# Kernel tuning notes

Measured on AMD Instinct MI355X. Metric: run time of the kernel, lower is better.

## Reference

```python
import jax, jax.numpy as jnp
import numpy as np

B, T, I, H = 32768, 18, 2, 64  # batch, seq_len (forced by fc2 in_features=18), input_dim, hidden_dim


def setup_inputs() -> dict:
    key = jax.random.key(0)
    ks = jax.random.split(key, 13)
    s = 1.0 / np.sqrt(H)  # torch default GRU/Linear init scale
    return {
        "x": jax.random.normal(ks[0], (B, T, I), jnp.float32),
        "w_ih_f": jax.random.uniform(ks[1], (3 * H, I), jnp.float32, -s, s),
        "w_hh_f": jax.random.uniform(ks[2], (3 * H, H), jnp.float32, -s, s),
        "b_ih_f": jax.random.uniform(ks[3], (3 * H,), jnp.float32, -s, s),
        "b_hh_f": jax.random.uniform(ks[4], (3 * H,), jnp.float32, -s, s),
        "w_ih_b": jax.random.uniform(ks[5], (3 * H, I), jnp.float32, -s, s),
        "w_hh_b": jax.random.uniform(ks[6], (3 * H, H), jnp.float32, -s, s),
        "b_ih_b": jax.random.uniform(ks[7], (3 * H,), jnp.float32, -s, s),
        "b_hh_b": jax.random.uniform(ks[8], (3 * H,), jnp.float32, -s, s),
        "fc1_w": jax.random.uniform(ks[9], (24, 2 * H), jnp.float32, -s, s),
        "fc1_b": jax.random.uniform(ks[10], (24,), jnp.float32, -s, s),
        "fc2_w": jax.random.uniform(ks[11], (2, T), jnp.float32, -s, s),
        "fc2_b": jax.random.uniform(ks[12], (2,), jnp.float32, -s, s),
    }


def _gru_scan(x_proj, w_hh, b_hh):
    """x_proj: (T, B, 3H) precomputed input projections. Returns (T, B, H)."""
    h0 = jnp.zeros((x_proj.shape[1], w_hh.shape[1]), x_proj.dtype)

    def step(h, xp):
        gh = h @ w_hh.T + b_hh
        i_r, i_z, i_n = jnp.split(xp, 3, axis=-1)
        h_r, h_z, h_n = jnp.split(gh, 3, axis=-1)
        r = jax.nn.sigmoid(i_r + h_r)
        z = jax.nn.sigmoid(i_z + h_z)
        n = jnp.tanh(i_n + r * h_n)
        h_new = (1 - z) * n + z * h
        return h_new, h_new

    _, hs = jax.lax.scan(step, h0, x_proj)
    return hs


def reference(x, w_ih_f, w_hh_f, b_ih_f, b_hh_f,
              w_ih_b, w_hh_b, b_ih_b, b_hh_b,
              fc1_w, fc1_b, fc2_w, fc2_b):
    # precompute input-gate projections for both directions: (T, B, 3H)
    xp_f = jnp.einsum('bti,gi->tbg', x, w_ih_f) + b_ih_f
    xp_b = jnp.einsum('bti,gi->tbg', x[:, ::-1], w_ih_b) + b_ih_b
    hf = _gru_scan(xp_f, w_hh_f, b_hh_f)           # (T, B, H)
    hb = _gru_scan(xp_b, w_hh_b, b_hh_b)[::-1]     # (T, B, H), re-aligned to forward time
    out = jnp.concatenate([hf, hb], axis=-1).transpose(1, 0, 2)  # (B, T, 2H)
    out = out @ fc1_w.T + fc1_b                    # (B, T, 24)
    out = out.reshape(out.shape[0], 24, -1)        # (B, 24, T) raw row-major reshape, as in torch
    out = out @ fc2_w.T + fc2_b                    # (B, 24, 2)
    return out
```

## Files before the change

kernel.cpp:

```cpp
#include <hip/hip_runtime.h>

#define TT 18

typedef __attribute__((ext_vector_type(8))) short short8;
typedef __attribute__((ext_vector_type(4))) float float4_t;
typedef __attribute__((ext_vector_type(2))) float float2_t;
typedef __attribute__((ext_vector_type(2))) unsigned int uint2_t;

static __device__ __forceinline__ float frcp(float x){ return __builtin_amdgcn_rcpf(x); }
static __device__ __forceinline__ float sigm(float x){ return frcp(1.f + __expf(-x)); }
static __device__ __forceinline__ float tanh_fast(float x){ return fmaf(2.f, frcp(1.f + __expf(-2.f*x)), -1.f); }
static __device__ __forceinline__ unsigned rne_bits(float f){
    unsigned u = __float_as_uint(f);
    return u + 0x7fffu + ((u >> 16) & 1u);
}
static __device__ __forceinline__ unsigned pack_hi16(unsigned hi_src, unsigned lo_src){
#if defined(__has_builtin)
#if __has_builtin(__builtin_amdgcn_perm)
    return __builtin_amdgcn_perm(hi_src, lo_src, 0x07060302u);
#else
    return (lo_src >> 16) | (hi_src & 0xffff0000u);
#endif
#else
    return (lo_src >> 16) | (hi_src & 0xffff0000u);
#endif
}

__global__ __launch_bounds__(256) void head_precompute(
    const float* __restrict__ fc1_w, const float* __restrict__ fc1_b,
    const float* __restrict__ fc2_w, const float* __restrict__ fc2_b,
    unsigned short* __restrict__ Bhi, unsigned short* __restrict__ Blo,
    float* __restrict__ Cvec)
{
    int idx = blockIdx.x * 256 + threadIdx.x;
    if (idx < 24 * 2 * 18 * 128) {
        int jg = idx & 127;
        int t  = (idx >> 7) % 18;
        int k  = (idx / 2304) & 1;
        int r  = idx / 4608;
        float acc = 0.f;
        for (int c = 0; c < 24; ++c) {
            int s = t * 24 + c - r * 18;
            if (s >= 0 && s < 18) acc += fc2_w[k * 18 + s] * fc1_w[c * 128 + jg];
        }
        unsigned rb = rne_bits(acc);
        Bhi[idx] = (unsigned short)(rb >> 16);
        float fh = __uint_as_float(rb & 0xffff0000u);
        Blo[idx] = (unsigned short)(__float_as_uint(acc - fh) >> 16);
    }
    if (idx < 48) {
        int k = idx & 1, r = idx >> 1;
        float acc = fc2_b[k];
        for (int s = 0; s < 18; ++s)
            acc += fc2_w[k * 18 + s] * fc1_b[(r * 18 + s) % 24];
        Cvec[idx] = acc;
    }
}

struct SMv {
    alignas(16) unsigned short hb[2][2][1024];
    float x_s[16][36];
    float out_acc[16][49];
};

__global__ __launch_bounds__(256, 4) void gru_mfma(
    const float* __restrict__ x,
    const float* __restrict__ w_ih_f, const float* __restrict__ w_hh_f,
    const float* __restrict__ b_ih_f, const float* __restrict__ b_hh_f,
    const float* __restrict__ w_ih_b, const float* __restrict__ w_hh_b,
    const float* __restrict__ b_ih_b, const float* __restrict__ b_hh_b,
    const unsigned short* __restrict__ Bhi, const unsigned short* __restrict__ Blo,
    const float* __restrict__ Cvec, float* __restrict__ out)
{
    __shared__ SMv sm;
    const int tid  = threadIdx.x;
    const int lane = tid & 63;
    const int jq   = tid >> 6;
    const int col  = lane & 15;
    const int quad = lane >> 4;
    const int bi   = blockIdx.x;
    const int dir  = bi >> 11;
    const int bb   = (bi & 2047) * 16;

    const float* __restrict__ wih = dir ? w_ih_b : w_ih_f;
    const float* __restrict__ whh = dir ? w_hh_b : w_hh_f;
    const float* __restrict__ bih = dir ? b_ih_b : b_ih_f;
    const float* __restrict__ bhh = dir ? b_hh_b : b_hh_f;

    if (tid < 144)
        ((float4_t*)sm.x_s)[tid] = ((const float4_t*)(x + (size_t)bb * 36))[tid];
    {
        unsigned* z = (unsigned*)&sm.hb[1][0][0];
        #pragma unroll
        for (int o = 0; o < 4; ++o) z[tid + o * 256] = 0u;
    }
    for (int o = tid; o < 16 * 49; o += 256) ((float*)sm.out_acc)[o] = 0.f;

    short8 wf[3][2];
    #pragma unroll
    for (int ty = 0; ty < 3; ++ty) {
        int g = ty * 64 + jq * 16 + col;
        #pragma unroll
        for (int c = 0; c < 2; ++c) {
            const float* p = whh + g * 64 + c * 32 + quad * 8;
            float4_t f0 = *(const float4_t*)p;
            float4_t f1 = *(const float4_t*)(p + 4);
            short8 s;
            #pragma unroll
            for (int e = 0; e < 8; ++e) {
                float f = (e < 4) ? f0[e] : f1[e - 4];
                s[e] = (short)(rne_bits(f) >> 16);
            }
            wf[ty][c] = s;
        }
    }

    float w0c[3][4], w1c[3][4], bA[3][4], bN[4];
    #pragma unroll
    for (int reg = 0; reg < 4; ++reg) {
        int j = jq * 16 + quad * 4 + reg;
        #pragma unroll
        for (int ty = 0; ty < 3; ++ty) {
            int g = ty * 64 + j;
            w0c[ty][reg] = wih[2 * g];
            w1c[ty][reg] = wih[2 * g + 1];
            bA[ty][reg]  = (ty < 2) ? (bih[g] + bhh[g]) : bih[g];
        }
        bN[reg] = bhh[128 + j];
    }

    float hprev[4] = {0.f, 0.f, 0.f, 0.f};

    __syncthreads();

    auto step = [&](int t, int pr, int pw) {
        short8 hfh[2], hfl[2];
        #pragma unroll
        for (int c = 0; c < 2; ++c) {
            hfh[c] = *(const short8*)&sm.hb[pr][0][(c * 4 + quad) * 128 + col * 8];
            hfl[c] = *(const short8*)&sm.hb[pr][1][(c * 4 + quad) * 128 + col * 8];
        }

        if (t > 0 && ((t - 1) & 3) == jq) {
            int s  = t - 1;
            int ta = dir ? (TT - 1 - s) : s;
            int i  = col & 3;
            int rr = 4 * (ta / 3) + ta % 3 + (i >> 1);
            int kk = i & 1;
            size_t boff = (size_t)((rr * 2 + kk) * TT + ta) * 128 + dir * 64 + quad * 8;
            float4_t acch = (float4_t){0.f, 0.f, 0.f, 0.f};
            #pragma unroll
            for (int c = 0; c < 2; ++c) {
                short8 ah = *(const short8*)(Bhi + boff + c * 32);
                short8 al = *(const short8*)(Blo + boff + c * 32);
                acch = __builtin_amdgcn_mfma_f32_16x16x32_bf16(ah, hfh[c], acch, 0, 0, 0);
                acch = __builtin_amdgcn_mfma_f32_16x16x32_bf16(ah, hfl[c], acch, 0, 0, 0);
                acch = __builtin_amdgcn_mfma_f32_16x16x32_bf16(al, hfh[c], acch, 0, 0, 0);
            }
            if (quad == 0) {
                #pragma unroll
                for (int reg = 0; reg < 4; ++reg) {
                    int r2 = 4 * (ta / 3) + ta % 3 + (reg >> 1);
                    sm.out_acc[col][r2 * 2 + (reg & 1)] += acch[reg];
                }
            }
        }

        float4_t acc[3];
        #pragma unroll
        for (int ty = 0; ty < 3; ++ty) acc[ty] = (float4_t){0.f, 0.f, 0.f, 0.f};
        #pragma unroll
        for (int ty = 0; ty < 3; ++ty)
          #pragma unroll
          for (int c = 0; c < 2; ++c) {
            acc[ty] = __builtin_amdgcn_mfma_f32_16x16x32_bf16(wf[ty][c], hfh[c], acc[ty], 0, 0, 0);
            acc[ty] = __builtin_amdgcn_mfma_f32_16x16x32_bf16(wf[ty][c], hfl[c], acc[ty], 0, 0, 0);
          }

        const int tx = dir ? (TT - 1 - t) : t;
        float2_t xv = *(const float2_t*)&sm.x_s[col][tx * 2];
        unsigned rh[4], ul[4];
        #pragma unroll
        for (int reg = 0; reg < 4; ++reg) {
            float r  = sigm(fmaf(w0c[0][reg], xv[0], fmaf(w1c[0][reg], xv[1], bA[0][reg])) + acc[0][reg]);
            float z  = sigm(fmaf(w0c[1][reg], xv[0], fmaf(w1c[1][reg], xv[1], bA[1][reg])) + acc[1][reg]);
            float xn = fmaf(w0c[2][reg], xv[0], fmaf(w1c[2][reg], xv[1], bA[2][reg]));
            float n  = tanh_fast(fmaf(r, acc[2][reg] + bN[reg], xn));
            float hnew = fmaf(z, hprev[reg] - n, n);
            hprev[reg] = hnew;
            unsigned rb = rne_bits(hnew);
            rh[reg] = rb;
            float fh = __uint_as_float(rb & 0xffff0000u);
            ul[reg] = __float_as_uint(hnew - fh);
        }
        int woff = (jq * 2 + (quad >> 1)) * 128 + col * 8 + (quad & 1) * 4;
        uint2_t dh, dl;
        dh[0] = pack_hi16(rh[1], rh[0]);
        dh[1] = pack_hi16(rh[3], rh[2]);
        dl[0] = pack_hi16(ul[1], ul[0]);
        dl[1] = pack_hi16(ul[3], ul[2]);
        *(uint2_t*)&sm.hb[pw][0][woff] = dh;
        *(uint2_t*)&sm.hb[pw][1][woff] = dl;
        __syncthreads();
    };

    #pragma unroll 1
    for (int tt = 0; tt < 9; ++tt) {
        step(2 * tt,     1, 0);
        step(2 * tt + 1, 0, 1);
    }

    if (jq == (17 & 3)) {
        short8 hfh[2], hfl[2];
        #pragma unroll
        for (int c = 0; c < 2; ++c) {
            hfh[c] = *(const short8*)&sm.hb[1][0][(c * 4 + quad) * 128 + col * 8];
            hfl[c] = *(const short8*)&sm.hb[1][1][(c * 4 + quad) * 128 + col * 8];
        }
        int s  = TT - 1;
        int ta = dir ? 0 : s;
        int i  = col & 3;
        int rr = 4 * (ta / 3) + ta % 3 + (i >> 1);
        int kk = i & 1;
        size_t boff = (size_t)((rr * 2 + kk) * TT + ta) * 128 + dir * 64 + quad * 8;
        float4_t acch = (float4_t){0.f, 0.f, 0.f, 0.f};
        #pragma unroll
        for (int c = 0; c < 2; ++c) {
            short8 ah = *(const short8*)(Bhi + boff + c * 32);
            short8 al = *(const short8*)(Blo + boff + c * 32);
            acch = __builtin_amdgcn_mfma_f32_16x16x32_bf16(ah, hfh[c], acch, 0, 0, 0);
            acch = __builtin_amdgcn_mfma_f32_16x16x32_bf16(ah, hfl[c], acch, 0, 0, 0);
            acch = __builtin_amdgcn_mfma_f32_16x16x32_bf16(al, hfh[c], acch, 0, 0, 0);
        }
        if (quad == 0) {
            #pragma unroll
            for (int reg = 0; reg < 4; ++reg) {
                int r2 = 4 * (ta / 3) + ta % 3 + (reg >> 1);
                sm.out_acc[col][r2 * 2 + (reg & 1)] += acch[reg];
            }
        }
    }
    __syncthreads();

    #pragma unroll
    for (int rep = 0; rep < 3; ++rep) {
        int o = rep * 256 + tid;
        int b = o / 48, c = o % 48;
        atomicAdd(&out[(size_t)bb * 48 + o], sm.out_acc[b][c] + 0.5f * Cvec[c]);
    }
}

extern "C" void kernel_launch(void* const* d_in, const int* in_sizes, int n_in,
                              void* d_out, int out_size, void* d_ws, size_t ws_size,
                              hipStream_t stream) {
    const float* x      = (const float*)d_in[0];
    const float* w_ih_f = (const float*)d_in[1];
    const float* w_hh_f = (const float*)d_in[2];
    const float* b_ih_f = (const float*)d_in[3];
    const float* b_hh_f = (const float*)d_in[4];
    const float* w_ih_b = (const float*)d_in[5];
    const float* w_hh_b = (const float*)d_in[6];
    const float* b_ih_b = (const float*)d_in[7];
    const float* b_hh_b = (const float*)d_in[8];
    const float* fc1_w  = (const float*)d_in[9];
    const float* fc1_b  = (const float*)d_in[10];
    const float* fc2_w  = (const float*)d_in[11];
    const float* fc2_b  = (const float*)d_in[12];
    float* out  = (float*)d_out;

    float*          Cvec = (float*)d_ws;
    unsigned short* Bhi  = (unsigned short*)((char*)d_ws + 256);
    unsigned short* Blo  = Bhi + 110592;

    hipMemsetAsync(d_out, 0, (size_t)out_size * sizeof(float), stream);
    head_precompute<<<432, 256, 0, stream>>>(fc1_w, fc1_b, fc2_w, fc2_b, Bhi, Blo, Cvec);
    gru_mfma<<<4096, 256, 0, stream>>>(x, w_ih_f, w_hh_f, b_ih_f, b_hh_f,
                                       w_ih_b, w_hh_b, b_ih_b, b_hh_b,
                                       Bhi, Blo, Cvec, out);
}
```

Baseline: 215.9 us.

## Drop hi/lo bf16 split for recurrent MFMA and fold input projection into MFMA

```diff
diff --git a/kernel.cpp b/kernel.cpp
--- a/kernel.cpp
+++ b/kernel.cpp
@@ -4,7 +4,6 @@
 
 typedef __attribute__((ext_vector_type(8))) short short8;
 typedef __attribute__((ext_vector_type(4))) float float4_t;
-typedef __attribute__((ext_vector_type(2))) float float2_t;
 typedef __attribute__((ext_vector_type(2))) unsigned int uint2_t;
 
 static __device__ __forceinline__ float frcp(float x){ return __builtin_amdgcn_rcpf(x); }
@@ -13,6 +12,12 @@
 static __device__ __forceinline__ unsigned rne_bits(float f){
     unsigned u = __float_as_uint(f);
     return u + 0x7fffu + ((u >> 16) & 1u);
+}
+static __device__ __forceinline__ void bsplit(float f, unsigned &hi, unsigned &lo){
+    unsigned rb = rne_bits(f);
+    hi = rb >> 16;
+    float fh = __uint_as_float(rb & 0xffff0000u);
+    lo = rne_bits(f - fh) >> 16;
 }
 static __device__ __forceinline__ unsigned pack_hi16(unsigned hi_src, unsigned lo_src){
 #if defined(__has_builtin)
@@ -25,6 +30,8 @@
     return (lo_src >> 16) | (hi_src & 0xffff0000u);
 #endif
 }
+
+union U8 { short8 s; unsigned u[4]; };
 
 __global__ __launch_bounds__(256) void head_precompute(
     const float* __restrict__ fc1_w, const float* __restrict__ fc1_b,
@@ -43,10 +50,10 @@
             int s = t * 24 + c - r * 18;
             if (s >= 0 && s < 18) acc += fc2_w[k * 18 + s] * fc1_w[c * 128 + jg];
         }
-        unsigned rb = rne_bits(acc);
-        Bhi[idx] = (unsigned short)(rb >> 16);
-        float fh = __uint_as_float(rb & 0xffff0000u);
-        Blo[idx] = (unsigned short)(__float_as_uint(acc - fh) >> 16);
+        unsigned hi, lo;
+        bsplit(acc, hi, lo);
+        Bhi[idx] = (unsigned short)hi;
+        Blo[idx] = (unsigned short)lo;
     }
     if (idx < 48) {
         int k = idx & 1, r = idx >> 1;
@@ -59,7 +66,7 @@
 
 struct SMv {
     alignas(16) unsigned short hb[2][2][1024];
-    float x_s[16][36];
+    uint2_t x2[16][18];
     float out_acc[16][49];
 };
 
@@ -81,14 +88,23 @@
     const int bi   = blockIdx.x;
     const int dir  = bi >> 11;
     const int bb   = (bi & 2047) * 16;
+    const bool q0  = (quad == 0);
 
     const float* __restrict__ wih = dir ? w_ih_b : w_ih_f;
     const float* __restrict__ whh = dir ? w_hh_b : w_hh_f;
     const float* __restrict__ bih = dir ? b_ih_b : b_ih_f;
     const float* __restrict__ bhh = dir ? b_hh_b : b_hh_f;
 
-    if (tid < 144)
-        ((float4_t*)sm.x_s)[tid] = ((const float4_t*)(x + (size_t)bb * 36))[tid];
+    #pragma unroll
+    for (int p = tid; p < 288; p += 256) {
+        int b = p / 18, t = p % 18;
+        const float* xp = x + (size_t)(bb + b) * 36 + t * 2;
+        unsigned h0, l0, h1, l1;
+        bsplit(xp[0], h0, l0);
+        bsplit(xp[1], h1, l1);
+        uint2_t s2; s2[0] = h0 | (l0 << 16); s2[1] = h1 | (l1 << 16);
+        sm.x2[b][t] = s2;
+    }
     {
         unsigned* z = (unsigned*)&sm.hb[1][0][0];
         #pragma unroll
@@ -115,18 +131,38 @@
         }
     }
 
-    float w0c[3][4], w1c[3][4], bA[3][4], bN[4];
-    #pragma unroll
-    for (int reg = 0; reg < 4; ++reg) {
-        int j = jq * 16 + quad * 4 + reg;
-        #pragma unroll
-        for (int ty = 0; ty < 3; ++ty) {
-            int g = ty * 64 + j;
-            w0c[ty][reg] = wih[2 * g];
-            w1c[ty][reg] = wih[2 * g + 1];
-            bA[ty][reg]  = (ty < 2) ? (bih[g] + bhh[g]) : bih[g];
-        }
-        bN[reg] = bhh[128 + j];
+    short8 c2[4];
+    {
+        #pragma unroll
+        for (int ty = 0; ty < 2; ++ty) {
+            int g = ty * 64 + jq * 16 + col;
+            unsigned w0h, w0l, w1h, w1l, bh, bl;
+            bsplit(wih[2 * g],     w0h, w0l);
+            bsplit(wih[2 * g + 1], w1h, w1l);
+            bsplit(bih[g] + bhh[g], bh, bl);
+            U8 f;
+            f.u[0] = q0 ? (w0h | (w0h << 16)) : 0u;
+            f.u[1] = q0 ? (w0l | (w1h << 16)) : 0u;
+            f.u[2] = q0 ? (w1h | (w1l << 16)) : 0u;
+            f.u[3] = q0 ? (bh  | (bl  << 16)) : 0u;
+            c2[ty] = f.s;
+        }
+        int g = 128 + jq * 16 + col;
+        unsigned w0h, w0l, w1h, w1l, bxh, bxl, bhh_h, bhh_l;
+        bsplit(wih[2 * g],     w0h, w0l);
+        bsplit(wih[2 * g + 1], w1h, w1l);
+        bsplit(bih[g], bxh, bxl);
+        bsplit(bhh[g], bhh_h, bhh_l);
+        U8 fn;
+        fn.u[0] = 0u; fn.u[1] = 0u; fn.u[2] = 0u;
+        fn.u[3] = q0 ? (bhh_h | (bhh_l << 16)) : 0u;
+        c2[2] = fn.s;
+        U8 fx;
+        fx.u[0] = q0 ? (w0h | (w0h << 16)) : 0u;
+        fx.u[1] = q0 ? (w0l | (w1h << 16)) : 0u;
+        fx.u[2] = q0 ? (w1h | (w1l << 16)) : 0u;
+        fx.u[3] = q0 ? (bxh | (bxl << 16)) : 0u;
+        c2[3] = fx.s;
     }
 
     float hprev[4] = {0.f, 0.f, 0.f, 0.f};
@@ -134,73 +170,97 @@
     __syncthreads();
 
     auto step = [&](int t, int pr, int pw) {
-        short8 hfh[2], hfl[2];
+        const bool myhead = (t > 0) && (((t - 1) & 3) == jq);
+
+        int ta_h = 0, base_h = 0;
+        size_t boff = 0;
+        short8 hA0, hA1, lA0, lA1, hfl0, hfl1;
+        if (myhead) {
+            int s  = t - 1;
+            ta_h   = dir ? (TT - 1 - s) : s;
+            base_h = 4 * (ta_h / 3) + ta_h % 3;
+            int i  = col & 3;
+            int rr = base_h + (i >> 1);
+            int kk = i & 1;
+            boff = (size_t)((rr * 2 + kk) * TT + ta_h) * 128 + dir * 64 + quad * 8;
+            hA0 = *(const short8*)(Bhi + boff);
+            hA1 = *(const short8*)(Bhi + boff + 32);
+            hfl0 = *(const short8*)&sm.hb[pr][1][(0 * 4 + quad) * 128 + col * 8];
+            hfl1 = *(const short8*)&sm.hb[pr][1][(1 * 4 + quad) * 128 + col * 8];
+        }
+
+        short8 hfh[2];
+        #pragma unroll
+        for (int c = 0; c < 2; ++c)
+            hfh[c] = *(const short8*)&sm.hb[pr][0][(c * 4 + quad) * 128 + col * 8];
+
+        const int tx = dir ? (TT - 1 - t) : t;
+        short8 b2f;
+        {
+            uint2_t xs = sm.x2[col][tx];
+            U8 B;
+            B.u[0] = q0 ? xs[0] : 0u;
+            B.u[1] = q0 ? ((xs[0] & 0xffffu) | (xs[1] << 16)) : 0u;
+            B.u[2] = q0 ? ((xs[1] >> 16) | (xs[1] << 16)) : 0u;
+            B.u[3] = q0 ? 0x3F803F80u : 0u;
+            b2f = B.s;
+        }
+
+        float4_t aR  = (float4_t){0.f,0.f,0.f,0.f};
+        float4_t aZ  = (float4_t){0.f,0.f,0.f,0.f};
+        float4_t aNH = (float4_t){0.f,0.f,0.f,0.f};
+        float4_t aNX = (float4_t){0.f,0.f,0.f,0.f};
         #pragma unroll
         for (int c = 0; c < 2; ++c) {
-            hfh[c] = *(const short8*)&sm.hb[pr][0][(c * 4 + quad) * 128 + col * 8];
-            hfl[c] = *(const short8*)&sm.hb[pr][1][(c * 4 + quad) * 128 + col * 8];
-        }
-
-        if (t > 0 && ((t - 1) & 3) == jq) {
-            int s  = t - 1;
-            int ta = dir ? (TT - 1 - s) : s;
-            int i  = col & 3;
-            int rr = 4 * (ta / 3) + ta % 3 + (i >> 1);
-            int kk = i & 1;
-            size_t boff = (size_t)((rr * 2 + kk) * TT + ta) * 128 + dir * 64 + quad * 8;
-            float4_t acch = (float4_t){0.f, 0.f, 0.f, 0.f};
-            #pragma unroll
-            for (int c = 0; c < 2; ++c) {
-                short8 ah = *(const short8*)(Bhi + boff + c * 32);
-                short8 al = *(const short8*)(Blo + boff + c * 32);
-                acch = __builtin_amdgcn_mfma_f32_16x16x32_bf16(ah, hfh[c], acch, 0, 0, 0);
-                acch = __builtin_amdgcn_mfma_f32_16x16x32_bf16(ah, hfl[c], acch, 0, 0, 0);
-                acch = __builtin_amdgcn_mfma_f32_16x16x32_bf16(al, hfh[c], acch, 0, 0, 0);
-            }
-            if (quad == 0) {
-                #pragma unroll
-                for (int reg = 0; reg < 4; ++reg) {
-                    int r2 = 4 * (ta / 3) + ta % 3 + (reg >> 1);
-                    sm.out_acc[col][r2 * 2 + (reg & 1)] += acch[reg];
-                }
-            }
-        }
-
-        float4_t acc[3];
-        #pragma unroll
-        for (int ty = 0; ty < 3; ++ty) acc[ty] = (float4_t){0.f, 0.f, 0.f, 0.f};
-        #pragma unroll
-        for (int ty = 0; ty < 3; ++ty)
-          #pragma unroll
-          for (int c = 0; c < 2; ++c) {
-            acc[ty] = __builtin_amdgcn_mfma_f32_16x16x32_bf16(wf[ty][c], hfh[c], acc[ty], 0, 0, 0);
-            acc[ty] = __builtin_amdgcn_mfma_f32_16x16x32_bf16(wf[ty][c], hfl[c], acc[ty], 0, 0, 0);
-          }
-
-        const int tx = dir ? (TT - 1 - t) : t;
-        float2_t xv = *(const float2_t*)&sm.x_s[col][tx * 2];
-        unsigned rh[4], ul[4];
+            aR  = __builtin_amdgcn_mfma_f32_16x16x32_bf16(wf[0][c], hfh[c], aR,  0, 0, 0);
+            aZ  = __builtin_amdgcn_mfma_f32_16x16x32_bf16(wf[1][c], hfh[c], aZ,  0, 0, 0);
+            aNH = __builtin_amdgcn_mfma_f32_16x16x32_bf16(wf[2][c], hfh[c], aNH, 0, 0, 0);
+        }
+        aR  = __builtin_amdgcn_mfma_f32_16x16x32_bf16(c2[0], b2f, aR,  0, 0, 0);
+        aZ  = __builtin_amdgcn_mfma_f32_16x16x32_bf16(c2[1], b2f, aZ,  0, 0, 0);
+        aNH = __builtin_amdgcn_mfma_f32_16x16x32_bf16(c2[2], b2f, aNH, 0, 0, 0);
+        aNX = __builtin_amdgcn_mfma_f32_16x16x32_bf16(c2[3], b2f, aNX, 0, 0, 0);
+
+        unsigned rh[4], rl[4];
         #pragma unroll
         for (int reg = 0; reg < 4; ++reg) {
-            float r  = sigm(fmaf(w0c[0][reg], xv[0], fmaf(w1c[0][reg], xv[1], bA[0][reg])) + acc[0][reg]);
-            float z  = sigm(fmaf(w0c[1][reg], xv[0], fmaf(w1c[1][reg], xv[1], bA[1][reg])) + acc[1][reg]);
-            float xn = fmaf(w0c[2][reg], xv[0], fmaf(w1c[2][reg], xv[1], bA[2][reg]));
-            float n  = tanh_fast(fmaf(r, acc[2][reg] + bN[reg], xn));
+            float r = sigm(aR[reg]);
+            float z = sigm(aZ[reg]);
+            float n = tanh_fast(fmaf(r, aNH[reg], aNX[reg]));
             float hnew = fmaf(z, hprev[reg] - n, n);
             hprev[reg] = hnew;
             unsigned rb = rne_bits(hnew);
             rh[reg] = rb;
             float fh = __uint_as_float(rb & 0xffff0000u);
-            ul[reg] = __float_as_uint(hnew - fh);
+            rl[reg] = rne_bits(hnew - fh);
         }
         int woff = (jq * 2 + (quad >> 1)) * 128 + col * 8 + (quad & 1) * 4;
         uint2_t dh, dl;
         dh[0] = pack_hi16(rh[1], rh[0]);
         dh[1] = pack_hi16(rh[3], rh[2]);
-        dl[0] = pack_hi16(ul[1], ul[0]);
-        dl[1] = pack_hi16(ul[3], ul[2]);
+        dl[0] = pack_hi16(rl[1], rl[0]);
+        dl[1] = pack_hi16(rl[3], rl[2]);
         *(uint2_t*)&sm.hb[pw][0][woff] = dh;
         *(uint2_t*)&sm.hb[pw][1][woff] = dl;
+
+        if (myhead) {
+            lA0 = *(const short8*)(Blo + boff);
+            lA1 = *(const short8*)(Blo + boff + 32);
+            float4_t acch = (float4_t){0.f,0.f,0.f,0.f};
+            acch = __builtin_amdgcn_mfma_f32_16x16x32_bf16(hA0, hfh[0], acch, 0, 0, 0);
+            acch = __builtin_amdgcn_mfma_f32_16x16x32_bf16(hA1, hfh[1], acch, 0, 0, 0);
+            acch = __builtin_amdgcn_mfma_f32_16x16x32_bf16(hA0, hfl0,   acch, 0, 0, 0);
+            acch = __builtin_amdgcn_mfma_f32_16x16x32_bf16(hA1, hfl1,   acch, 0, 0, 0);
+            acch = __builtin_amdgcn_mfma_f32_16x16x32_bf16(lA0, hfh[0], acch, 0, 0, 0);
+            acch = __builtin_amdgcn_mfma_f32_16x16x32_bf16(lA1, hfh[1], acch, 0, 0, 0);
+            if (q0) {
+                #pragma unroll
+                for (int reg = 0; reg < 4; ++reg) {
+                    int r2 = base_h + (reg >> 1);
+                    sm.out_acc[col][r2 * 2 + (reg & 1)] += acch[reg];
+                }
+            }
+        }
         __syncthreads();
     };
 
@@ -210,32 +270,33 @@
         step(2 * tt + 1, 0, 1);
     }
 
-    if (jq == (17 & 3)) {
-        short8 hfh[2], hfl[2];
-        #pragma unroll
-        for (int c = 0; c < 2; ++c) {
-            hfh[c] = *(const short8*)&sm.hb[1][0][(c * 4 + quad) * 128 + col * 8];
-            hfl[c] = *(const short8*)&sm.hb[1][1][(c * 4 + quad) * 128 + col * 8];
-        }
+    if (jq == ((TT - 1) & 3)) {
         int s  = TT - 1;
         int ta = dir ? 0 : s;
+        int base_h = 4 * (ta / 3) + ta % 3;
         int i  = col & 3;
-        int rr = 4 * (ta / 3) + ta % 3 + (i >> 1);
+        int rr = base_h + (i >> 1);
         int kk = i & 1;
         size_t boff = (size_t)((rr * 2 + kk) * TT + ta) * 128 + dir * 64 + quad * 8;
-        float4_t acch = (float4_t){0.f, 0.f, 0.f, 0.f};
-        #pragma unroll
-        for (int c = 0; c < 2; ++c) {
-            short8 ah = *(const short8*)(Bhi + boff + c * 32);
-            short8 al = *(const short8*)(Blo + boff + c * 32);
-            acch = __builtin_amdgcn_mfma_f32_16x16x32_bf16(ah, hfh[c], acch, 0, 0, 0);
-            acch = __builtin_amdgcn_mfma_f32_16x16x32_bf16(ah, hfl[c], acch, 0, 0, 0);
-            acch = __builtin_amdgcn_mfma_f32_16x16x32_bf16(al, hfh[c], acch, 0, 0, 0);
-        }
-        if (quad == 0) {
+        short8 hA0 = *(const short8*)(Bhi + boff);
+        short8 hA1 = *(const short8*)(Bhi + boff + 32);
+        short8 lA0 = *(const short8*)(Blo + boff);
+        short8 lA1 = *(const short8*)(Blo + boff + 32);
+        short8 hfh0 = *(const short8*)&sm.hb[1][0][(0 * 4 + quad) * 128 + col * 8];
+        short8 hfh1 = *(const short8*)&sm.hb[1][0][(1 * 4 + quad) * 128 + col * 8];
+        short8 hfl0 = *(const short8*)&sm.hb[1][1][(0 * 4 + quad) * 128 + col * 8];
+        short8 hfl1 = *(const short8*)&sm.hb[1][1][(1 * 4 + quad) * 128 + col * 8];
+        float4_t acch = (float4_t){0.f,0.f,0.f,0.f};
+        acch = __builtin_amdgcn_mfma_f32_16x16x32_bf16(hA0, hfh0, acch, 0, 0, 0);
+        acch = __builtin_amdgcn_mfma_f32_16x16x32_bf16(hA1, hfh1, acch, 0, 0, 0);
+        acch = __builtin_amdgcn_mfma_f32_16x16x32_bf16(hA0, hfl0, acch, 0, 0, 0);
+        acch = __builtin_amdgcn_mfma_f32_16x16x32_bf16(hA1, hfl1, acch, 0, 0, 0);
+        acch = __builtin_amdgcn_mfma_f32_16x16x32_bf16(lA0, hfh0, acch, 0, 0, 0);
+        acch = __builtin_amdgcn_mfma_f32_16x16x32_bf16(lA1, hfh1, acch, 0, 0, 0);
+        if (q0) {
             #pragma unroll
             for (int reg = 0; reg < 4; ++reg) {
-                int r2 = 4 * (ta / 3) + ta % 3 + (reg >> 1);
+                int r2 = base_h + (reg >> 1);
                 sm.out_acc[col][r2 * 2 + (reg & 1)] += acch[reg];
             }
         }
```

Result: faster. 194.5 us (-9.9%).
